# Kernel optimization log

Measured on AMD Instinct MI355X. Metric: run time of the kernel, lower is better.

Reference implementation:

```python
import jax, jax.numpy as jnp
import numpy as np


def setup_inputs() -> dict:
    key = jax.random.key(0)
    k1, k2, k3, k4, k5 = jax.random.split(key, 5)
    B, Ci, Co, H, W, N, K = 8, 256, 256, 128, 128, 4, 3
    x = jax.random.normal(k1, (B, Ci, H, W), dtype=jnp.float32)
    weight = jax.random.normal(k2, (N, Co, Ci, K, K), dtype=jnp.float32)
    styles = jax.random.normal(k3, (B, Ci), dtype=jnp.float32)
    selector = jax.random.uniform(k4, (B, N), dtype=jnp.float32)
    noise = jax.random.normal(k5, (B, Co, H, W), dtype=jnp.float32)
    return {"x": x, "weight": weight, "styles": styles,
            "selector": selector, "noise": noise}


def reference(x, weight, styles, selector, noise):
    """Modulated conv2d with adaptive kernel selection (fused_modconv path).

    x:        [B, Ci, H, W]
    weight:   [N, Co, Ci, kh, kw]  kernel bank
    styles:   [B, Ci]              modulation
    selector: [B, N]               adaptive kernel mixing coefficients
    noise:    [B, Co, H, W]        additive noise
    """
    B, Ci, H, W = x.shape
    N, Co, _, kh, kw = weight.shape

    # adaptive kernel selection: per-sample kernel = selector-weighted sum of bank
    w = jnp.einsum('bn,noihw->boihw', selector, weight)          # [B,Co,Ci,kh,kw]

    # modulate by styles
    w = w * styles[:, None, :, None, None]

    # demodulate
    dcoefs = jax.lax.rsqrt(jnp.sum(w * w, axis=(2, 3, 4)) + 1e-8)  # [B,Co]
    w = w * dcoefs[:, :, None, None, None]

    # fused per-sample conv via grouped conv (groups = B), cross-correlation
    # (flip_weight=True in the torch code means plain conv2d / cross-correlation)
    xr = x.reshape(1, B * Ci, H, W)
    wr = w.reshape(B * Co, Ci, kh, kw)
    out = jax.lax.conv_general_dilated(
        xr, wr,
        window_strides=(1, 1),
        padding=[(kh // 2, kh // 2), (kw // 2, kw // 2)],
        feature_group_count=B,
        dimension_numbers=('NCHW', 'OIHW', 'NCHW'),
    )
    out = out.reshape(B, Co, H, W) + noise
    return out
```

## Files before the change

### kernel.cpp

```cpp
#include <hip/hip_runtime.h>


typedef __attribute__((ext_vector_type(4))) float f32x4;
typedef __attribute__((ext_vector_type(8))) short s16x8;

#define NB   8
#define NCI  256
#define NCO  256
#define NHW  128
#define NKER 4

#define SB0 __builtin_amdgcn_sched_barrier(0)
#define BAR __builtin_amdgcn_s_barrier()
#define WAITL0 asm volatile("s_waitcnt lgkmcnt(0)" ::: "memory")

__device__ __forceinline__ unsigned short f2bf(float f) {
  unsigned int u = __builtin_bit_cast(unsigned int, f);
  u += 0x7FFFu + ((u >> 16) & 1u);
  return (unsigned short)(u >> 16);
}

__global__ __launch_bounds__(256) void prep_k(
    const float* __restrict__ weight,
    const float* __restrict__ styles,
    const float* __restrict__ selector,
    unsigned short* __restrict__ wmod)
{
  int bid = blockIdx.x;
  int b = bid >> 8, co = bid & 255;
  int ci = threadIdx.x;

  float sel[NKER];
#pragma unroll
  for (int n = 0; n < NKER; ++n) sel[n] = selector[b * NKER + n];

  float a[9];
#pragma unroll
  for (int j = 0; j < 9; ++j) a[j] = 0.f;
#pragma unroll
  for (int n = 0; n < NKER; ++n) {
    const float* wp = weight + (size_t)((n * NCO + co) * NCI + ci) * 9;
    float s = sel[n];
#pragma unroll
    for (int j = 0; j < 9; ++j) a[j] += s * wp[j];
  }
  float st = styles[b * NCI + ci];
  float ss = 0.f;
#pragma unroll
  for (int j = 0; j < 9; ++j) { a[j] *= st; ss += a[j] * a[j]; }

  for (int off = 32; off; off >>= 1) ss += __shfl_down(ss, off, 64);
  __shared__ float red[4];
  int wid = threadIdx.x >> 6, lane = threadIdx.x & 63;
  if (lane == 0) red[wid] = ss;
  __syncthreads();
  float tot = red[0] + red[1] + red[2] + red[3];
  float d = rsqrtf(tot + 1e-8f);

  int kb = ci >> 5;
  size_t base = (size_t)(co >> 4) * 512 +
                (size_t)(((ci & 31) >> 3) * 128) + ((co & 15) * 8) + (ci & 7);
#pragma unroll
  for (int j = 0; j < 9; ++j) {
    size_t T = (size_t)((b * 9 + j) * 8 + kb);
    wmod[(T << 13) + base] = f2bf(a[j] * d);
  }
}

__global__ __launch_bounds__(256, 2) void conv_k(
    const float* __restrict__ x,
    const unsigned short* __restrict__ wg,
    const float* __restrict__ noise,
    float* __restrict__ out)
{
  extern __shared__ __align__(16) char XRs[];

  int orig = blockIdx.x;
  int b = orig & 7;
  int h = orig >> 3;

  int t = threadIdx.x;
  int lane = t & 63;
  int wid = t >> 6;
  int wr = wid >> 1, wc = wid & 1;
  int ll = lane & 15;
  int ks = lane >> 4;

  f32x4 acc[8][4];
#pragma unroll
  for (int m = 0; m < 8; ++m)
#pragma unroll
    for (int n = 0; n < 4; ++n) acc[m][n] = (f32x4){0.f, 0.f, 0.f, 0.f};

  int c = ((t >> 4) & 15) * 2;
  int wi = t & 15;
  float xlo[8], xhi[8];
  unsigned xmask = 0xFFFFFFFFu;

  auto issueX = [&](int g) {
    int gc = g < 24 ? g : 23;
    int dh = gc >> 3, kb = gc & 7;
    int hy = h + dh - 1;
    xmask = ((unsigned)hy < 128u) ? 0xFFFFFFFFu : 0u;
    int hyc = hy < 0 ? 0 : (hy > 127 ? 127 : hy);
    const float* base = x + ((size_t)(b * NCI + kb * 32 + c) * NHW + hyc) * NHW + wi;
#pragma unroll
    for (int j2 = 0; j2 < 8; ++j2) {
      xlo[j2] = base[j2 * 16];
      xhi[j2] = base[NHW * NHW + j2 * 16];
    }
  };

  auto issueAF = [&](int tc, s16x8* af) {
    if (tc > 71) tc = 71;
    int g = tc / 3, tap = tc - g * 3;
    int dh = g >> 3, kb = g & 7;
    const char* src = (const char*)wg +
        ((size_t)((b * 9 + dh * 3 + tap) * 8 + kb) << 14) +
        wr * 8192 + lane * 16;
#pragma unroll
    for (int m = 0; m < 8; ++m)
      af[m] = *(const s16x8*)(src + m * 1024);
  };

  auto packXR = [&](int g) {
    char* dstb = XRs + (g & 1) * 8192;
    int slot = (((wi & 1) << 2) + (c >> 3)) ^ ((wi >> 1) & 7);
    char* p0 = dstb + (wi >> 1) * 128 + (slot << 4) + ((c & 7) << 1);
#pragma unroll
    for (int j2 = 0; j2 < 8; ++j2) {
      unsigned pk = ((unsigned)f2bf(xhi[j2]) << 16) | f2bf(xlo[j2]);
      *(unsigned*)(p0 + j2 * 1024) = pk & xmask;
    }
  };

#define PFB(XRBASE, DW, bf)                                              \
  {                                                                      \
    const char* Xb = (XRBASE);                                           \
    _Pragma("unroll")                                                    \
    for (int n = 0; n < 4; ++n) {                                        \
      int wn = wc * 64 + n * 16 + ll + (DW) - 1;                         \
      if (((DW) == 0 && n == 0) || ((DW) == 2 && n == 3)) {              \
        int wx = wn < 0 ? 0 : (wn > 127 ? 127 : wn);                     \
        int row = wx >> 1;                                               \
        int slot = (((wx & 1) << 2) + ks) ^ (row & 7);                   \
        s16x8 bv = *(const s16x8*)(Xb + row * 128 + (slot << 4));        \
        if (wn != wx) { s16x8 z = {0, 0, 0, 0, 0, 0, 0, 0}; bv = z; }    \
        bf[n] = bv;                                                      \
      } else {                                                           \
        int row = wn >> 1;                                               \
        int slot = (((wn & 1) << 2) + ks) ^ (row & 7);                   \
        bf[n] = *(const s16x8*)(Xb + row * 128 + (slot << 4));           \
      }                                                                  \
    }                                                                    \
  }

#define MFMA32(af, bf)                                                   \
  __builtin_amdgcn_s_setprio(1);                                         \
  _Pragma("unroll")                                                      \
  for (int m = 0; m < 8; ++m)                                            \
    _Pragma("unroll")                                                    \
    for (int n = 0; n < 4; ++n)                                          \
      acc[m][n] = __builtin_amdgcn_mfma_f32_16x16x32_bf16(               \
          af[m], bf[n], acc[m][n], 0, 0, 0);                             \
  __builtin_amdgcn_s_setprio(0);

  s16x8 afA[8], afB[8], bf[4];

  issueX(0); SB0;
  issueAF(0, afA); SB0;
  packXR(0);

#pragma unroll 1
  for (int gg = 0; gg < 12; ++gg) {
    int g0 = gg * 2, t0 = gg * 6;
    WAITL0; SB0; BAR; SB0;
    PFB(XRs, 0, bf);
    issueAF(t0 + 1, afB); SB0;
    issueX(g0 + 1); SB0;
    MFMA32(afA, bf);
    PFB(XRs, 1, bf);
    issueAF(t0 + 2, afA); SB0;
    MFMA32(afB, bf);
    PFB(XRs, 2, bf);
    issueAF(t0 + 3, afB); SB0;
    packXR(g0 + 1);
    MFMA32(afA, bf);
    WAITL0; SB0; BAR; SB0;
    PFB(XRs + 8192, 0, bf);
    issueAF(t0 + 4, afA); SB0;
    issueX(g0 + 2); SB0;
    MFMA32(afB, bf);
    PFB(XRs + 8192, 1, bf);
    issueAF(t0 + 5, afB); SB0;
    MFMA32(afA, bf);
    PFB(XRs + 8192, 2, bf);
    issueAF(t0 + 6, afA); SB0;
    packXR(g0 + 2);
    MFMA32(afB, bf);
  }

  int pr4 = ks * 4;
#pragma unroll
  for (int m = 0; m < 8; ++m) {
#pragma unroll
    for (int n = 0; n < 4; ++n) {
      int px = wc * 64 + n * 16 + ll;
#pragma unroll
      for (int j = 0; j < 4; ++j) {
        int co = wr * 128 + m * 16 + pr4 + j;
        size_t idx = ((size_t)(b * NCO + co) * NHW + h) * NHW + px;
        out[idx] = acc[m][n][j] + noise[idx];
      }
    }
  }
}

extern "C" void kernel_launch(void* const* d_in, const int* in_sizes, int n_in,
                              void* d_out, int out_size, void* d_ws, size_t ws_size,
                              hipStream_t stream) {
  const float* x        = (const float*)d_in[0];
  const float* weight   = (const float*)d_in[1];
  const float* styles   = (const float*)d_in[2];
  const float* selector = (const float*)d_in[3];
  const float* noise    = (const float*)d_in[4];
  float* out = (float*)d_out;

  unsigned short* wmod = (unsigned short*)d_ws;

  hipLaunchKernelGGL(prep_k, dim3(NB * NCO), dim3(256), 0, stream,
                     weight, styles, selector, wmod);
  hipLaunchKernelGGL(conv_k, dim3(NB * NHW), dim3(256), 16 * 1024, stream,
                     x, wmod, noise, out);
}
```

Baseline: 201.8 us.

## Split output channels across two blocks and shift LDS layout to drop edge clamps

Each block now computes half of the output channels (128 instead of 256) for one row, which doubles the grid and halves the accumulator registers so launch bounds can allow three blocks per CU. The X staging layout in LDS is shifted by one pixel with an extra row and a shared zero region, so boundary reads become an address redirect instead of a clamp plus select. The cost is that each X row is now loaded and converted twice, once by each channel-half block, which doubles the global X traffic and the bf16 packing work.

```diff
diff --git a/kernel.cpp b/kernel.cpp
--- a/kernel.cpp
+++ b/kernel.cpp
@@ -9,6 +9,8 @@
 #define NCO  256
 #define NHW  128
 #define NKER 4
+#define XRSTRIDE 8320
+#define ZOFF     16640
 
 #define SB0 __builtin_amdgcn_sched_barrier(0)
 #define BAR __builtin_amdgcn_s_barrier()
@@ -67,7 +69,7 @@
   }
 }
 
-__global__ __launch_bounds__(256, 2) void conv_k(
+__global__ __launch_bounds__(256, 3) void conv_k(
     const float* __restrict__ x,
     const unsigned short* __restrict__ wg,
     const float* __restrict__ noise,
@@ -77,7 +79,9 @@
 
   int orig = blockIdx.x;
   int b = orig & 7;
-  int h = orig >> 3;
+  int r0 = orig >> 3;
+  int h = r0 >> 1;
+  int cot = r0 & 1;
 
   int t = threadIdx.x;
   int lane = t & 63;
@@ -86,15 +90,15 @@
   int ll = lane & 15;
   int ks = lane >> 4;
 
-  f32x4 acc[8][4];
-#pragma unroll
-  for (int m = 0; m < 8; ++m)
+  f32x4 acc[4][4];
+#pragma unroll
+  for (int m = 0; m < 4; ++m)
 #pragma unroll
     for (int n = 0; n < 4; ++n) acc[m][n] = (f32x4){0.f, 0.f, 0.f, 0.f};
 
   int c = ((t >> 4) & 15) * 2;
-  int wi = t & 15;
-  float xlo[8], xhi[8];
+  int j = t & 15;
+  float xA0[5], xB0[5], xA1[5], xB1[5];
   unsigned xmask = 0xFFFFFFFFu;
 
   auto issueX = [&](int g) {
@@ -103,11 +107,19 @@
     int hy = h + dh - 1;
     xmask = ((unsigned)hy < 128u) ? 0xFFFFFFFFu : 0u;
     int hyc = hy < 0 ? 0 : (hy > 127 ? 127 : hy);
-    const float* base = x + ((size_t)(b * NCI + kb * 32 + c) * NHW + hyc) * NHW + wi;
-#pragma unroll
-    for (int j2 = 0; j2 < 8; ++j2) {
-      xlo[j2] = base[j2 * 16];
-      xhi[j2] = base[NHW * NHW + j2 * 16];
+    const float* b0 = x + ((size_t)(b * NCI + kb * 32 + c) * NHW + hyc) * NHW;
+    const float* b1 = b0 + NHW * NHW;
+#pragma unroll
+    for (int k = 0; k < 4; ++k) {
+      int rr = j + 16 * k;
+      int wA = 2 * rr - 1; if (wA < 0) wA = 0;
+      int wB = 2 * rr;
+      xA0[k] = b0[wA]; xB0[k] = b0[wB];
+      xA1[k] = b1[wA]; xB1[k] = b1[wB];
+    }
+    if (j == 0) {
+      xA0[4] = b0[127]; xB0[4] = b0[127];
+      xA1[4] = b1[127]; xB1[4] = b1[127];
     }
   };
 
@@ -117,56 +129,68 @@
     int dh = g >> 3, kb = g & 7;
     const char* src = (const char*)wg +
         ((size_t)((b * 9 + dh * 3 + tap) * 8 + kb) << 14) +
-        wr * 8192 + lane * 16;
-#pragma unroll
-    for (int m = 0; m < 8; ++m)
+        cot * 8192 + wr * 4096 + lane * 16;
+#pragma unroll
+    for (int m = 0; m < 4; ++m)
       af[m] = *(const s16x8*)(src + m * 1024);
   };
 
   auto packXR = [&](int g) {
-    char* dstb = XRs + (g & 1) * 8192;
-    int slot = (((wi & 1) << 2) + (c >> 3)) ^ ((wi >> 1) & 7);
-    char* p0 = dstb + (wi >> 1) * 128 + (slot << 4) + ((c & 7) << 1);
-#pragma unroll
-    for (int j2 = 0; j2 < 8; ++j2) {
-      unsigned pk = ((unsigned)f2bf(xhi[j2]) << 16) | f2bf(xlo[j2]);
-      *(unsigned*)(p0 + j2 * 1024) = pk & xmask;
+    char* dstb = XRs + (g & 1) * XRSTRIDE;
+    int cg = c >> 3, cb = (c & 7) << 1;
+#pragma unroll
+    for (int k = 0; k < 4; ++k) {
+      int rr = j + 16 * k;
+      int s0 = (cg) ^ (rr & 7);
+      int s1 = (4 + cg) ^ (rr & 7);
+      unsigned p0 = ((unsigned)f2bf(xA1[k]) << 16) | f2bf(xA0[k]);
+      unsigned p1 = ((unsigned)f2bf(xB1[k]) << 16) | f2bf(xB0[k]);
+      *(unsigned*)(dstb + rr * 128 + s0 * 16 + cb) = p0 & xmask;
+      *(unsigned*)(dstb + rr * 128 + s1 * 16 + cb) = p1 & xmask;
+    }
+    if (j == 0) {
+      int s0 = cg;
+      int s1 = 4 + cg;
+      unsigned p0 = ((unsigned)f2bf(xA1[4]) << 16) | f2bf(xA0[4]);
+      unsigned p1 = ((unsigned)f2bf(xB1[4]) << 16) | f2bf(xB0[4]);
+      *(unsigned*)(dstb + 64 * 128 + s0 * 16 + cb) = p0 & xmask;
+      *(unsigned*)(dstb + 64 * 128 + s1 * 16 + cb) = p1 & xmask;
     }
   };
 
-#define PFB(XRBASE, DW, bf)                                              \
+#define RDB(BUFOFF, DW, n, dst)                                          \
   {                                                                      \
-    const char* Xb = (XRBASE);                                           \
+    int wn = wc * 64 + (n) * 16 + ll + (DW) - 1;                         \
+    int wp1 = wn + 1;                                                    \
+    int row = wp1 >> 1;                                                  \
+    int slot = (((wp1 & 1) << 2) + ks) ^ (row & 7);                      \
+    int a = (BUFOFF) + row * 128 + (slot << 4);                          \
+    if (((DW) == 0 && (n) == 0) || ((DW) == 2 && (n) == 3)) {            \
+      if ((unsigned)wn > 127u) a = ZOFF + (ks << 4);                     \
+    }                                                                    \
+    dst = *(const s16x8*)(XRs + a);                                      \
+  }
+
+#define PFB(BUFOFF, DW, bf)                                              \
+  {                                                                      \
     _Pragma("unroll")                                                    \
-    for (int n = 0; n < 4; ++n) {                                        \
-      int wn = wc * 64 + n * 16 + ll + (DW) - 1;                         \
-      if (((DW) == 0 && n == 0) || ((DW) == 2 && n == 3)) {              \
-        int wx = wn < 0 ? 0 : (wn > 127 ? 127 : wn);                     \
-        int row = wx >> 1;                                               \
-        int slot = (((wx & 1) << 2) + ks) ^ (row & 7);                   \
-        s16x8 bv = *(const s16x8*)(Xb + row * 128 + (slot << 4));        \
-        if (wn != wx) { s16x8 z = {0, 0, 0, 0, 0, 0, 0, 0}; bv = z; }    \
-        bf[n] = bv;                                                      \
-      } else {                                                           \
-        int row = wn >> 1;                                               \
-        int slot = (((wn & 1) << 2) + ks) ^ (row & 7);                   \
-        bf[n] = *(const s16x8*)(Xb + row * 128 + (slot << 4));           \
-      }                                                                  \
-    }                                                                    \
-  }
-
-#define MFMA32(af, bf)                                                   \
+    for (int n = 0; n < 4; ++n) RDB(BUFOFF, DW, n, bf[n]);               \
+  }
+
+#define MFMA16(af, bf)                                                   \
   __builtin_amdgcn_s_setprio(1);                                         \
   _Pragma("unroll")                                                      \
-  for (int m = 0; m < 8; ++m)                                            \
+  for (int m = 0; m < 4; ++m)                                            \
     _Pragma("unroll")                                                    \
     for (int n = 0; n < 4; ++n)                                          \
       acc[m][n] = __builtin_amdgcn_mfma_f32_16x16x32_bf16(               \
           af[m], bf[n], acc[m][n], 0, 0, 0);                             \
   __builtin_amdgcn_s_setprio(0);
 
-  s16x8 afA[8], afB[8], bf[4];
-
+  s16x8 afA[4], afB[4], bf[4];
+
+  if (t < 16)
+    *(f32x4*)(XRs + ZOFF + t * 16) = (f32x4){0.f, 0.f, 0.f, 0.f};
   issueX(0); SB0;
   issueAF(0, afA); SB0;
   packXR(0);
@@ -175,42 +199,42 @@
   for (int gg = 0; gg < 12; ++gg) {
     int g0 = gg * 2, t0 = gg * 6;
     WAITL0; SB0; BAR; SB0;
-    PFB(XRs, 0, bf);
+    PFB(0, 0, bf);
     issueAF(t0 + 1, afB); SB0;
     issueX(g0 + 1); SB0;
-    MFMA32(afA, bf);
-    PFB(XRs, 1, bf);
+    MFMA16(afA, bf);
+    PFB(0, 1, bf);
     issueAF(t0 + 2, afA); SB0;
-    MFMA32(afB, bf);
-    PFB(XRs, 2, bf);
+    MFMA16(afB, bf);
+    PFB(0, 2, bf);
     issueAF(t0 + 3, afB); SB0;
     packXR(g0 + 1);
-    MFMA32(afA, bf);
+    MFMA16(afA, bf);
     WAITL0; SB0; BAR; SB0;
-    PFB(XRs + 8192, 0, bf);
+    PFB(XRSTRIDE, 0, bf);
     issueAF(t0 + 4, afA); SB0;
     issueX(g0 + 2); SB0;
-    MFMA32(afB, bf);
-    PFB(XRs + 8192, 1, bf);
+    MFMA16(afB, bf);
+    PFB(XRSTRIDE, 1, bf);
     issueAF(t0 + 5, afB); SB0;
-    MFMA32(afA, bf);
-    PFB(XRs + 8192, 2, bf);
+    MFMA16(afA, bf);
+    PFB(XRSTRIDE, 2, bf);
     issueAF(t0 + 6, afA); SB0;
     packXR(g0 + 2);
-    MFMA32(afB, bf);
+    MFMA16(afB, bf);
   }
 
   int pr4 = ks * 4;
 #pragma unroll
-  for (int m = 0; m < 8; ++m) {
+  for (int m = 0; m < 4; ++m) {
 #pragma unroll
     for (int n = 0; n < 4; ++n) {
       int px = wc * 64 + n * 16 + ll;
 #pragma unroll
-      for (int j = 0; j < 4; ++j) {
-        int co = wr * 128 + m * 16 + pr4 + j;
+      for (int jj = 0; jj < 4; ++jj) {
+        int co = cot * 128 + wr * 64 + m * 16 + pr4 + jj;
         size_t idx = ((size_t)(b * NCO + co) * NHW + h) * NHW + px;
-        out[idx] = acc[m][n][j] + noise[idx];
+        out[idx] = acc[m][n][jj] + noise[idx];
       }
     }
   }
@@ -230,6 +254,6 @@
 
   hipLaunchKernelGGL(prep_k, dim3(NB * NCO), dim3(256), 0, stream,
                      weight, styles, selector, wmod);
-  hipLaunchKernelGGL(conv_k, dim3(NB * NHW), dim3(256), 16 * 1024, stream,
+  hipLaunchKernelGGL(conv_k, dim3(NB * 2 * NHW), dim3(256), 16896, stream,
                      x, wmod, noise, out);
 }
```

Result: slower. 330.0 us (+63.5%).
